# Kernel optimization log

Hardware: AMD Instinct MI355X
Metric: run time of the kernel (lower is better)

The kernel has to match this reference:

```python
import jax, jax.numpy as jnp
import numpy as np

B, L = 512, 16

def setup_inputs() -> dict:
    key = jax.random.key(0)
    k1, k2 = jax.random.split(key)
    y_true = jax.random.randint(k1, (B, L), 0, 2, dtype=jnp.int32)
    y_pred = jax.random.normal(k2, (B, L), dtype=jnp.float32)
    return {"y_true": y_true, "y_pred": y_pred}

def reference(y_true, y_pred):
    b = y_true.shape[0]
    yt = y_true.reshape(b, -1)
    yp = y_pred.reshape(b, -1)
    l = yp.shape[1]
    mp = (yt == 1).astype(yp.dtype)          # [B,L] positive-row mask per label
    mn = 1.0 - mp                             # [B,L] negative-row mask per label
    n_pos = mp.sum(axis=0)                    # [L]
    n_neg = mn.sum(axis=0)                    # [L]
    # Torch selects FULL rows for pos/neg then flattens, so for each label the
    # hinge pairs every element of a positive row with every element of a
    # negative row. S[i,j] = sum_{c,d} relu(1 - yp[i,c] + yp[j,d]) is shared
    # across labels; only the row masks differ per label.
    T = jax.nn.relu(1.0 - yp[:, :, None, None] + yp[None, None, :, :])  # [B,L,B,L]
    S = T.sum(axis=(1, 3))                    # [B,B]
    per_label = jnp.einsum('il,ij,jl->l', mp, S, mn)  # sum over pos rows i, neg rows j
    # weight * mean = (1/(np*nn)) * sum / (np*L * nn*L) = sum / (np^2 * nn^2 * L^2)
    denom = (n_pos * n_neg) ** 2 * (l * l)
    valid = (n_pos > 0) & (n_neg > 0)
    loss = jnp.sum(jnp.where(valid, per_label / jnp.where(valid, denom, 1.0), 0.0))
    return loss
```

## Files before the change

### kernel.cpp

```cpp
#include <hip/hip_runtime.h>

#define NROWS 512
#define NLAB  16
#define TILE  16
#define GRIDX (NROWS / TILE)
#define NBLK  (GRIDX * GRIDX)

__global__ __launch_bounds__(256) void auc_single(const int* __restrict__ yt,
                                                  const float* __restrict__ yp,
                                                  float* __restrict__ out) {
    __shared__ float ya[TILE][TILE];
    __shared__ float yb[TILE][TILE];
    __shared__ float S_tile[TILE][TILE + 1];
    __shared__ unsigned posA[TILE];
    __shared__ unsigned posB[TILE];
    __shared__ int   lcnt[16][NLAB];
    __shared__ float wsum[NLAB];

    const int bx = blockIdx.x;
    const int i0 = (bx >> 5) * TILE;
    const int j0 = (bx & 31) * TILE;
    const int t  = threadIdx.x;
    const int r  = t >> 4;
    const int c  = t & 15;

    ya[r][c] = yp[(i0 + r) * NLAB + c];
    yb[r][c] = yp[(j0 + r) * NLAB + c] + 1.0f;
    {
        unsigned long long ba = __ballot(yt[(i0 + r) * NLAB + c] == 1);
        unsigned long long bb = __ballot(yt[(j0 + r) * NLAB + c] == 1);
        if (c == 0) {
            posA[r] = (unsigned)((ba >> ((r & 3) * 16)) & 0xFFFFull);
            posB[r] = (unsigned)((bb >> ((r & 3) * 16)) & 0xFFFFull);
        }
    }

    int cnt = 0;
    #pragma unroll 8
    for (int k = 0; k < NROWS / 16; ++k) {
        cnt += (yt[(r + 16 * k) * NLAB + c] == 1) ? 1 : 0;
    }
    __syncthreads();

    float a[TILE], b[TILE];
    #pragma unroll
    for (int k = 0; k < TILE; ++k) a[k] = ya[r][k];
    #pragma unroll
    for (int k = 0; k < TILE; ++k) b[k] = yb[c][k];

    float S = 0.0f;
    #pragma unroll
    for (int d = 0; d < TILE; ++d) {
        #pragma unroll
        for (int cc = 0; cc < TILE; ++cc) {
            S += fmaxf(b[d] - a[cc], 0.0f);
        }
    }
    S_tile[r][c] = S;
    lcnt[r][c] = cnt;
    __syncthreads();

    const int l = r, ti = c;
    float rowsum = 0.0f;
    #pragma unroll
    for (int tj = 0; tj < TILE; ++tj) {
        if (((~posB[tj]) >> l) & 1u) rowsum += S_tile[ti][tj];
    }
    float val = ((posA[ti] >> l) & 1u) ? rowsum : 0.0f;
    val += __shfl_xor(val, 1);
    val += __shfl_xor(val, 2);
    val += __shfl_xor(val, 4);
    val += __shfl_xor(val, 8);

    if (c == 0) {
        int np_ = 0;
        #pragma unroll
        for (int g = 0; g < 16; ++g) np_ += lcnt[g][r];
        const int nn_ = NROWS - np_;
        float w = 0.0f;
        if (np_ > 0 && nn_ > 0) {
            const double prod = (double)np_ * (double)nn_;
            w = (float)((double)val / (prod * prod * (double)(NLAB * NLAB)));
        }
        wsum[r] = w;
    }
    __syncthreads();

    if (t == 0) {
        float s = 0.0f;
        #pragma unroll
        for (int g = 0; g < NLAB; ++g) s += wsum[g];
        atomicAdd(out, s);
    }
}

extern "C" void kernel_launch(void* const* d_in, const int* in_sizes, int n_in,
                              void* d_out, int out_size, void* d_ws, size_t ws_size,
                              hipStream_t stream) {
    const int* y_true = (const int*)d_in[0];
    const float* y_pred = (const float*)d_in[1];
    float* out = (float*)d_out;

    auc_single<<<NBLK, 256, 0, stream>>>(y_true, y_pred, out);
}
```

Measured before the change: 71.15 us.

## Loop each block over eight j-tiles to cut block count and atomics

Reduces the grid from 1024 blocks to 128. Each block keeps its i-tile in registers and iterates over 8 j-tiles using double-buffered shared tiles, accumulating per-label sums before a single atomicAdd. This amortizes the per-block label-count scan, the weight computation and the atomics over more work. The cost is less parallelism (128 blocks on a large GPU) and serial syncs within each block.

```diff
diff --git a/kernel.cpp b/kernel.cpp
--- a/kernel.cpp
+++ b/kernel.cpp
@@ -3,93 +3,105 @@
 #define NROWS 512
 #define NLAB  16
 #define TILE  16
-#define GRIDX (NROWS / TILE)
-#define NBLK  (GRIDX * GRIDX)
+#define NTJ   8
+#define NBLKS 128
 
 __global__ __launch_bounds__(256) void auc_single(const int* __restrict__ yt,
                                                   const float* __restrict__ yp,
                                                   float* __restrict__ out) {
     __shared__ float ya[TILE][TILE];
-    __shared__ float yb[TILE][TILE];
-    __shared__ float S_tile[TILE][TILE + 1];
+    __shared__ float yb[2][TILE][TILE];
+    __shared__ float S_tile[2][TILE][TILE + 1];
     __shared__ unsigned posA[TILE];
-    __shared__ unsigned posB[TILE];
+    __shared__ unsigned posB[2][TILE];
     __shared__ int   lcnt[16][NLAB];
-    __shared__ float wsum[NLAB];
+    __shared__ float wfac[NLAB];
+    __shared__ float lsumf[NLAB];
 
     const int bx = blockIdx.x;
-    const int i0 = (bx >> 5) * TILE;
-    const int j0 = (bx & 31) * TILE;
+    const int i0 = (bx >> 2) * TILE;
+    const int jb = (bx & 3) * NTJ;
     const int t  = threadIdx.x;
     const int r  = t >> 4;
     const int c  = t & 15;
 
     ya[r][c] = yp[(i0 + r) * NLAB + c];
-    yb[r][c] = yp[(j0 + r) * NLAB + c] + 1.0f;
     {
         unsigned long long ba = __ballot(yt[(i0 + r) * NLAB + c] == 1);
-        unsigned long long bb = __ballot(yt[(j0 + r) * NLAB + c] == 1);
-        if (c == 0) {
-            posA[r] = (unsigned)((ba >> ((r & 3) * 16)) & 0xFFFFull);
-            posB[r] = (unsigned)((bb >> ((r & 3) * 16)) & 0xFFFFull);
-        }
+        if (c == 0) posA[r] = (unsigned)((ba >> ((r & 3) * 16)) & 0xFFFFull);
     }
-
     int cnt = 0;
     #pragma unroll 8
     for (int k = 0; k < NROWS / 16; ++k) {
         cnt += (yt[(r + 16 * k) * NLAB + c] == 1) ? 1 : 0;
     }
-    __syncthreads();
-
-    float a[TILE], b[TILE];
-    #pragma unroll
-    for (int k = 0; k < TILE; ++k) a[k] = ya[r][k];
-    #pragma unroll
-    for (int k = 0; k < TILE; ++k) b[k] = yb[c][k];
-
-    float S = 0.0f;
-    #pragma unroll
-    for (int d = 0; d < TILE; ++d) {
-        #pragma unroll
-        for (int cc = 0; cc < TILE; ++cc) {
-            S += fmaxf(b[d] - a[cc], 0.0f);
-        }
-    }
-    S_tile[r][c] = S;
     lcnt[r][c] = cnt;
     __syncthreads();
 
-    const int l = r, ti = c;
-    float rowsum = 0.0f;
-    #pragma unroll
-    for (int tj = 0; tj < TILE; ++tj) {
-        if (((~posB[tj]) >> l) & 1u) rowsum += S_tile[ti][tj];
-    }
-    float val = ((posA[ti] >> l) & 1u) ? rowsum : 0.0f;
-    val += __shfl_xor(val, 1);
-    val += __shfl_xor(val, 2);
-    val += __shfl_xor(val, 4);
-    val += __shfl_xor(val, 8);
-
-    if (c == 0) {
+    if (t < NLAB) {
         int np_ = 0;
         #pragma unroll
-        for (int g = 0; g < 16; ++g) np_ += lcnt[g][r];
+        for (int g = 0; g < 16; ++g) np_ += lcnt[g][t];
         const int nn_ = NROWS - np_;
         float w = 0.0f;
         if (np_ > 0 && nn_ > 0) {
             const double prod = (double)np_ * (double)nn_;
-            w = (float)((double)val / (prod * prod * (double)(NLAB * NLAB)));
+            w = (float)(1.0 / (prod * prod * (double)(NLAB * NLAB)));
         }
-        wsum[r] = w;
+        wfac[t] = w;
     }
+
+    float a[TILE];
+    #pragma unroll
+    for (int k = 0; k < TILE; ++k) a[k] = ya[r][k];
+
+    float acc = 0.0f;
+
+    for (int k = 0; k < NTJ; ++k) {
+        const int p  = k & 1;
+        const int j0 = (jb + k) * TILE;
+
+        yb[p][r][c] = yp[(j0 + r) * NLAB + c] + 1.0f;
+        {
+            unsigned long long bb = __ballot(yt[(j0 + r) * NLAB + c] == 1);
+            if (c == 0) posB[p][r] = (unsigned)((bb >> ((r & 3) * 16)) & 0xFFFFull);
+        }
+        __syncthreads();
+
+        float b[TILE];
+        #pragma unroll
+        for (int q = 0; q < TILE; ++q) b[q] = yb[p][c][q];
+
+        float S = 0.0f;
+        #pragma unroll
+        for (int d = 0; d < TILE; ++d) {
+            #pragma unroll
+            for (int cc = 0; cc < TILE; ++cc) {
+                S += fmaxf(b[d] - a[cc], 0.0f);
+            }
+        }
+        S_tile[p][r][c] = S;
+        __syncthreads();
+
+        float rowsum = 0.0f;
+        #pragma unroll
+        for (int tj = 0; tj < TILE; ++tj) {
+            if (((~posB[p][tj]) >> r) & 1u) rowsum += S_tile[p][c][tj];
+        }
+        float val = ((posA[c] >> r) & 1u) ? rowsum : 0.0f;
+        val += __shfl_xor(val, 1);
+        val += __shfl_xor(val, 2);
+        val += __shfl_xor(val, 4);
+        val += __shfl_xor(val, 8);
+        acc += val;
+    }
+
+    if (c == 0) lsumf[r] = acc * wfac[r];
     __syncthreads();
-
     if (t == 0) {
         float s = 0.0f;
         #pragma unroll
-        for (int g = 0; g < NLAB; ++g) s += wsum[g];
+        for (int g = 0; g < NLAB; ++g) s += lsumf[g];
         atomicAdd(out, s);
     }
 }
@@ -101,5 +113,5 @@
     const float* y_pred = (const float*)d_in[1];
     float* out = (float*)d_out;
 
-    auc_single<<<NBLK, 256, 0, stream>>>(y_true, y_pred, out);
+    auc_single<<<NBLKS, 256, 0, stream>>>(y_true, y_pred, out);
 }
```

After: 79.34 us. 1.12x slower.
